# Kernel tuning notes

Measured on AMD Instinct MI355X. Metric: run time of the kernel, lower is better.

## Reference

```python
import jax, jax.numpy as jnp
import numpy as np

D_MODEL = 1024
HEAD = 16


def setup_inputs() -> dict:
    key = jax.random.key(0)
    ks = jax.random.split(key, 11)
    B, S, D = 2, 2048, D_MODEL
    s = 1.0 / np.sqrt(D)
    return {
        "query": jax.random.normal(ks[0], (B, S, D), jnp.float32),
        "value": jax.random.normal(ks[1], (B, S, D), jnp.float32),
        "key": jax.random.normal(ks[2], (B, S, D), jnp.float32),
        "Wq_w": jax.random.normal(ks[3], (D, D), jnp.float32) * s,
        "Wq_b": jnp.zeros((D,), jnp.float32),
        "Wk_w": jax.random.normal(ks[4], (D, D), jnp.float32) * s,
        "Wk_b": jnp.zeros((D,), jnp.float32),
        "Wv_w": jax.random.normal(ks[5], (D, D), jnp.float32) * s,
        "Wv_b": jnp.zeros((D,), jnp.float32),
        "Wo_w": jax.random.normal(ks[6], (D, D), jnp.float32) * s,
        "Wo_b": jnp.zeros((D,), jnp.float32),
    }


def reference(query, value, key, Wq_w, Wq_b, Wk_w, Wk_b, Wv_w, Wv_b, Wo_w, Wo_b):
    B, S, D = query.shape
    H = HEAD
    kd = D // H
    # Linear projections (torch Linear: x @ W.T + b)
    Q = query @ Wq_w.T + Wq_b
    K = key @ Wk_w.T + Wk_b
    V = value @ Wv_w.T + Wv_b
    # [B, S, D] -> [B, H, S, kd]
    Q = Q.reshape(B, S, H, kd).transpose(0, 2, 1, 3)
    K = K.reshape(B, S, H, kd).transpose(0, 2, 1, 3)
    V = V.reshape(B, S, H, kd).transpose(0, 2, 1, 3)
    scale = 1.0 / jnp.sqrt(jnp.asarray(kd, query.dtype))
    score = jnp.einsum("bhqd,bhkd->bhqk", Q, K) * scale  # [B,H,S,S]
    attn = jax.nn.softmax(score, axis=-1)
    x = jnp.einsum("bhqk,bhkd->bhqd", attn, V)  # [B,H,S,kd]
    x = x.transpose(0, 2, 1, 3).reshape(B, S, D)
    return x @ Wo_w.T + Wo_b
```

## Files before the change

kernel.cpp:

```cpp
#include <hip/hip_runtime.h>
#include <stdint.h>
#include <stddef.h>


typedef __attribute__((ext_vector_type(8))) short short8;
typedef __attribute__((ext_vector_type(4))) float floatx4;
typedef __attribute__((ext_vector_type(16))) float f32x16;
typedef __attribute__((ext_vector_type(4))) unsigned short ushort4v;

#define MFMA16(a, b, c) __builtin_amdgcn_mfma_f32_16x16x32_bf16((a), (b), (c), 0, 0, 0)
#define MFMA32(a, b, c) __builtin_amdgcn_mfma_f32_32x32x16_bf16((a), (b), (c), 0, 0, 0)

#define CL2 0.18033688011112042f

__device__ __forceinline__ unsigned short f2bf(float f) {
  union { float f; unsigned u; } v; v.f = f;
  unsigned u = v.u;
  return (unsigned short)((u + 0x7fffu + ((u >> 16) & 1u)) >> 16);
}

__device__ __forceinline__ float fast_exp2(float x) {
  float r;
  asm("v_exp_f32 %0, %1" : "=v"(r) : "v"(x));
  return r;
}

__device__ __forceinline__ unsigned cvt_pk_bf16(float lo, float hi) {
  unsigned r;
  asm("v_cvt_pk_bf16_f32 %0, %1, %2" : "=v"(r) : "v"(lo), "v"(hi));
  return r;
}

#define PSWAP(a, b) asm("v_permlane32_swap_b32 %0, %1" : "+v"(a), "+v"(b))

union B8 { unsigned short s[8]; short8 v; };
union U4 { unsigned w[4]; short8 v; };

__device__ __forceinline__ void gload_lds16(const unsigned short* g, unsigned short* l) {
  __builtin_amdgcn_global_load_lds(
      (__attribute__((address_space(1))) void*)(g),
      (__attribute__((address_space(3))) void*)(l), 16, 0, 0);
}

__global__ __launch_bounds__(256) void convert_all(
    const float* __restrict__ q, const float* __restrict__ k, const float* __restrict__ v,
    const float* __restrict__ wq, const float* __restrict__ wk,
    const float* __restrict__ wv, const float* __restrict__ wo,
    unsigned short* __restrict__ qb, unsigned short* __restrict__ kb,
    unsigned short* __restrict__ vb, unsigned short* __restrict__ w4)
{
  int b = blockIdx.x;
  const float* s; unsigned short* d;
  float sc = 1.0f;
  if (b < 2048)      { s = q;  d = qb; }
  else if (b < 4096) { s = k;  d = kb; b -= 2048; }
  else if (b < 6144) { s = v;  d = vb; b -= 4096; }
  else if (b < 6656) { s = wq; d = w4;            b -= 6144; sc = CL2; }
  else if (b < 7168) { s = wk; d = w4 + 1048576;  b -= 6656; }
  else if (b < 7680) { s = wv; d = w4 + 2097152;  b -= 7168; }
  else               { s = wo; d = w4 + 3145728;  b -= 7680; }
  const size_t i = ((size_t)b * 256 + threadIdx.x) * 8;
  float4 f0 = *(const float4*)(s + i);
  float4 f1 = *(const float4*)(s + i + 4);
  B8 u;
  u.s[0] = f2bf(f0.x * sc); u.s[1] = f2bf(f0.y * sc);
  u.s[2] = f2bf(f0.z * sc); u.s[3] = f2bf(f0.w * sc);
  u.s[4] = f2bf(f1.x * sc); u.s[5] = f2bf(f1.y * sc);
  u.s[6] = f2bf(f1.z * sc); u.s[7] = f2bf(f1.w * sc);
  *(short8*)(d + i) = u.v;
}

__global__ __launch_bounds__(256) void proj_gemm(
    const unsigned short* __restrict__ A0, const unsigned short* __restrict__ A1,
    const unsigned short* __restrict__ A2, const unsigned short* __restrict__ W4,
    const float* __restrict__ b0, const float* __restrict__ b1, const float* __restrict__ b2,
    unsigned short* __restrict__ Qp, unsigned short* __restrict__ Kp,
    unsigned short* __restrict__ Vt)
{
  const int z = blockIdx.z;
  const unsigned short* A = (z == 0) ? A0 : ((z == 1) ? A1 : A2);
  const unsigned short* W = W4 + (size_t)z * 1048576;
  const float* bias = (z == 0) ? b0 : ((z == 1) ? b1 : b2);
  const float esc = (z == 0) ? CL2 : 1.0f;

  const int m0 = blockIdx.y * 128;
  const int n0 = blockIdx.x * 128;
  const int tid = threadIdx.x;
  const int lane = tid & 63;
  const int wid = tid >> 6;
  const int wr = wid >> 1, wc = wid & 1;
  const int g = lane >> 4, l15 = lane & 15;

  __shared__ unsigned short As[2][128 * 32];
  __shared__ unsigned short Bs[2][128 * 32];

  const floatx4 vzero = {0.f, 0.f, 0.f, 0.f};
  floatx4 acc[4][4];
#pragma unroll
  for (int i = 0; i < 4; ++i)
#pragma unroll
    for (int j = 0; j < 4; ++j) acc[i][j] = vzero;

  const int lr = lane >> 2;
  const int lc = (lane & 3) * 8;
  const unsigned short* pa = &A[(size_t)(m0 + lr) * 1024 + lc];
  const unsigned short* pw = &W[(size_t)(n0 + lr) * 1024 + lc];

#pragma unroll
  for (int t = 0; t < 2; ++t) {
    const int rb = (t * 4 + wid) * 16;
    gload_lds16(pa + (size_t)rb * 1024, &As[0][rb * 32]);
    gload_lds16(pw + (size_t)rb * 1024, &Bs[0][rb * 32]);
  }
  __syncthreads();

  int cur = 0;
  for (int k0 = 0; k0 < 1024; k0 += 32) {
    if (k0 + 32 < 1024) {
#pragma unroll
      for (int t = 0; t < 2; ++t) {
        const int rb = (t * 4 + wid) * 16;
        gload_lds16(pa + (size_t)rb * 1024 + k0 + 32, &As[cur ^ 1][rb * 32]);
        gload_lds16(pw + (size_t)rb * 1024 + k0 + 32, &Bs[cur ^ 1][rb * 32]);
      }
    }

    short8 af[4], bfr[4];
#pragma unroll
    for (int mt = 0; mt < 4; ++mt)
      af[mt] = *(const short8*)&As[cur][(wr * 64 + mt * 16 + l15) * 32 + g * 8];
#pragma unroll
    for (int nt = 0; nt < 4; ++nt)
      bfr[nt] = *(const short8*)&Bs[cur][(wc * 64 + nt * 16 + l15) * 32 + g * 8];

    __builtin_amdgcn_s_setprio(1);
#pragma unroll
    for (int mt = 0; mt < 4; ++mt)
#pragma unroll
      for (int nt = 0; nt < 4; ++nt)
        acc[mt][nt] = MFMA16(af[mt], bfr[nt], acc[mt][nt]);
    __builtin_amdgcn_s_setprio(0);

    __syncthreads();
    cur ^= 1;
  }

  float bvv[4];
#pragma unroll
  for (int nt = 0; nt < 4; ++nt) bvv[nt] = bias[n0 + wc * 64 + nt * 16 + l15] * esc;

  if (z < 2) {
    unsigned short* dst = (z == 0) ? Qp : Kp;
#pragma unroll
    for (int mt = 0; mt < 4; ++mt)
#pragma unroll
      for (int r = 0; r < 4; ++r) {
        const size_t row = (size_t)(m0 + wr * 64 + mt * 16 + g * 4 + r);
#pragma unroll
        for (int nt = 0; nt < 4; ++nt)
          dst[row * 1024 + n0 + wc * 64 + nt * 16 + l15] =
              f2bf(acc[mt][nt][r] + bvv[nt]);
      }
  } else {
#pragma unroll
    for (int mt = 0; mt < 4; ++mt) {
      const int sr = m0 + wr * 64 + mt * 16 + g * 4;
      const int bb = sr >> 11;
      const int ss = sr & 2047;
#pragma unroll
      for (int nt = 0; nt < 4; ++nt) {
        const int n = n0 + wc * 64 + nt * 16 + l15;
        const int hh = n >> 6, dd = n & 63;
        ushort4v o;
#pragma unroll
        for (int r = 0; r < 4; ++r) o[r] = f2bf(acc[mt][nt][r] + bvv[nt]);
        *(ushort4v*)&Vt[((size_t)(bb * 16 + hh) * 64 + dd) * 2048 + ss] = o;
      }
    }
  }
}

__global__ __launch_bounds__(256) void attn_kernel(
    const unsigned short* __restrict__ Qp, const unsigned short* __restrict__ Kp,
    const unsigned short* __restrict__ Vt, unsigned short* __restrict__ X)
{
  const int qb = blockIdx.x;
  const int bh = blockIdx.y;
  const int b = bh >> 4, h = bh & 15;
  const int tid = threadIdx.x, lane = tid & 63, w = tid >> 6;
  const int l31 = lane & 31, hi = lane >> 5;

  __shared__ unsigned short KV[2][2][4096];

  const int qrow = b * 2048 + qb * 128 + w * 32 + l31;
  short8 Qf[4];
#pragma unroll
  for (int ks = 0; ks < 4; ++ks)
    Qf[ks] = *(const short8*)&Qp[(size_t)qrow * 1024 + h * 64 + ks * 16 + hi * 8];

  const int s0 = tid, s1 = tid + 256;
  const int r0 = s0 >> 3, g0 = (s0 & 7) ^ (r0 & 7);
  const int r1 = s1 >> 3, g1 = (s1 & 7) ^ (r1 & 7);
  const unsigned short* kq0 = Kp + (size_t)(b * 2048 + r0) * 1024 + h * 64 + g0 * 8;
  const unsigned short* kq1 = Kp + (size_t)(b * 2048 + r1) * 1024 + h * 64 + g1 * 8;
  const unsigned short* vq0 = Vt + (size_t)(bh * 64 + r0) * 2048 + g0 * 8;
  const unsigned short* vq1 = Vt + (size_t)(bh * 64 + r1) * 2048 + g1 * 8;
  const int db0 = (w * 64) * 8;
  const int db1 = (256 + w * 64) * 8;

  f32x16 o0, o1;
#pragma unroll
  for (int i = 0; i < 16; ++i) { o0[i] = 0.f; o1[i] = 0.f; }
  float l_run = 0.f;

  gload_lds16(kq0, &KV[0][0][db0]);
  gload_lds16(kq1, &KV[0][0][db1]);
  gload_lds16(vq0, &KV[0][1][db0]);
  gload_lds16(vq1, &KV[0][1][db1]);
  __syncthreads();

  int cur = 0;
  for (int t = 0; t < 32; ++t) {
    if (t + 1 < 32) {
      const size_t ko = (size_t)(t + 1) * 65536;
      const size_t vo = (size_t)(t + 1) * 64;
      gload_lds16(kq0 + ko, &KV[cur ^ 1][0][db0]);
      gload_lds16(kq1 + ko, &KV[cur ^ 1][0][db1]);
      gload_lds16(vq0 + vo, &KV[cur ^ 1][1][db0]);
      gload_lds16(vq1 + vo, &KV[cur ^ 1][1][db1]);
    }
    const unsigned short* Kb = &KV[cur][0][0];
    const unsigned short* Vb = &KV[cur][1][0];

    f32x16 c0, c1;
#pragma unroll
    for (int i = 0; i < 16; ++i) { c0[i] = 0.f; c1[i] = 0.f; }
    __builtin_amdgcn_s_setprio(1);
    {
      const int base = l31 * 64, kx = l31 & 7;
#pragma unroll
      for (int ks = 0; ks < 4; ++ks) {
        const short8 kf = *(const short8*)&Kb[base + (((ks * 2 + hi) ^ kx) << 3)];
        c0 = MFMA32(kf, Qf[ks], c0);
      }
    }
    {
      const int krow = 32 + l31;
      const int base = krow * 64, kx = krow & 7;
#pragma unroll
      for (int ks = 0; ks < 4; ++ks) {
        const short8 kf = *(const short8*)&Kb[base + (((ks * 2 + hi) ^ kx) << 3)];
        c1 = MFMA32(kf, Qf[ks], c1);
      }
    }
    __builtin_amdgcn_s_setprio(0);

    short8 vf0[4], vf1[4];
#pragma unroll
    for (int ks = 0; ks < 4; ++ks) {
      const int vx0 = l31 & 7;
      vf0[ks] = *(const short8*)&Vb[l31 * 64 + (((ks * 2 + hi) ^ vx0) << 3)];
      const int vrow = 32 + l31;
      vf1[ks] = *(const short8*)&Vb[vrow * 64 + (((ks * 2 + hi) ^ (vrow & 7)) << 3)];
    }

#pragma unroll
    for (int i = 0; i < 16; ++i) { c0[i] = fast_exp2(c0[i]); l_run += c0[i]; }
#pragma unroll
    for (int i = 0; i < 16; ++i) { c1[i] = fast_exp2(c1[i]); l_run += c1[i]; }

    short8 PA0, PA1, PA2, PA3;
    {
      unsigned p0 = cvt_pk_bf16(c0[0], c0[1]),   p1 = cvt_pk_bf16(c0[2], c0[3]);
      unsigned p2 = cvt_pk_bf16(c0[4], c0[5]),   p3 = cvt_pk_bf16(c0[6], c0[7]);
      unsigned p4 = cvt_pk_bf16(c0[8], c0[9]),   p5 = cvt_pk_bf16(c0[10], c0[11]);
      unsigned p6 = cvt_pk_bf16(c0[12], c0[13]), p7 = cvt_pk_bf16(c0[14], c0[15]);
      PSWAP(p0, p2); PSWAP(p1, p3); PSWAP(p4, p6); PSWAP(p5, p7);
      U4 a, bb_;
      a.w[0] = p0; a.w[1] = p1; a.w[2] = p2; a.w[3] = p3;          PA0 = a.v;
      bb_.w[0] = p4; bb_.w[1] = p5; bb_.w[2] = p6; bb_.w[3] = p7;  PA1 = bb_.v;
    }
    {
      unsigned p0 = cvt_pk_bf16(c1[0], c1[1]),   p1 = cvt_pk_bf16(c1[2], c1[3]);
      unsigned p2 = cvt_pk_bf16(c1[4], c1[5]),   p3 = cvt_pk_bf16(c1[6], c1[7]);
      unsigned p4 = cvt_pk_bf16(c1[8], c1[9]),   p5 = cvt_pk_bf16(c1[10], c1[11]);
      unsigned p6 = cvt_pk_bf16(c1[12], c1[13]), p7 = cvt_pk_bf16(c1[14], c1[15]);
      PSWAP(p0, p2); PSWAP(p1, p3); PSWAP(p4, p6); PSWAP(p5, p7);
      U4 a, bb_;
      a.w[0] = p0; a.w[1] = p1; a.w[2] = p2; a.w[3] = p3;          PA2 = a.v;
      bb_.w[0] = p4; bb_.w[1] = p5; bb_.w[2] = p6; bb_.w[3] = p7;  PA3 = bb_.v;
    }

    __builtin_amdgcn_s_setprio(1);
#pragma unroll
    for (int ks = 0; ks < 4; ++ks) {
      const short8 pa = (ks == 0) ? PA0 : (ks == 1) ? PA1 : (ks == 2) ? PA2 : PA3;
      o0 = MFMA32(vf0[ks], pa, o0);
      o1 = MFMA32(vf1[ks], pa, o1);
    }
    __builtin_amdgcn_s_setprio(0);

    __syncthreads();
    cur ^= 1;
  }

  const float l_tot = l_run + __shfl_xor(l_run, 32);
  const float linv = 1.f / l_tot;
#pragma unroll
  for (int a = 0; a < 4; ++a) {
    ushort4v v0, v1;
#pragma unroll
    for (int r = 0; r < 4; ++r) {
      v0[r] = f2bf(o0[a * 4 + r] * linv);
      v1[r] = f2bf(o1[a * 4 + r] * linv);
    }
    *(ushort4v*)&X[(size_t)qrow * 1024 + h * 64 + a * 8 + hi * 4] = v0;
    *(ushort4v*)&X[(size_t)qrow * 1024 + h * 64 + 32 + a * 8 + hi * 4] = v1;
  }
}

__global__ __launch_bounds__(256) void out_gemm(
    const unsigned short* __restrict__ A, const unsigned short* __restrict__ W,
    const float* __restrict__ bias, float* __restrict__ out)
{
  const int m0 = blockIdx.y * 64;
  const int n0 = blockIdx.x * 128;
  const int tid = threadIdx.x;
  const int lane = tid & 63;
  const int wid = tid >> 6;
  const int wr = wid >> 1, wc = wid & 1;
  const int g = lane >> 4, l15 = lane & 15;

  __shared__ unsigned short As[2][64 * 32];
  __shared__ unsigned short Bs[2][128 * 32];

  const floatx4 vzero = {0.f, 0.f, 0.f, 0.f};
  floatx4 acc[2][4];
#pragma unroll
  for (int i = 0; i < 2; ++i)
#pragma unroll
    for (int j = 0; j < 4; ++j) acc[i][j] = vzero;

  const int lr = lane >> 2;
  const int lc = (lane & 3) * 8;
  const unsigned short* pa = &A[(size_t)(m0 + lr) * 1024 + lc];
  const unsigned short* pw = &W[(size_t)(n0 + lr) * 1024 + lc];

#pragma unroll
  for (int t = 0; t < 2; ++t) {
    const int rb = (t * 4 + wid) * 16;
    gload_lds16(pw + (size_t)rb * 1024, &Bs[0][rb * 32]);
  }
  gload_lds16(pa + (size_t)(wid * 16) * 1024, &As[0][wid * 16 * 32]);
  __syncthreads();

  int cur = 0;
  for (int k0 = 0; k0 < 1024; k0 += 32) {
    if (k0 + 32 < 1024) {
#pragma unroll
      for (int t = 0; t < 2; ++t) {
        const int rb = (t * 4 + wid) * 16;
        gload_lds16(pw + (size_t)rb * 1024 + k0 + 32, &Bs[cur ^ 1][rb * 32]);
      }
      gload_lds16(pa + (size_t)(wid * 16) * 1024 + k0 + 32, &As[cur ^ 1][wid * 16 * 32]);
    }

    short8 af[2], bfr[4];
#pragma unroll
    for (int mt = 0; mt < 2; ++mt)
      af[mt] = *(const short8*)&As[cur][(wr * 32 + mt * 16 + l15) * 32 + g * 8];
#pragma unroll
    for (int nt = 0; nt < 4; ++nt)
      bfr[nt] = *(const short8*)&Bs[cur][(wc * 64 + nt * 16 + l15) * 32 + g * 8];

    __builtin_amdgcn_s_setprio(1);
#pragma unroll
    for (int mt = 0; mt < 2; ++mt)
#pragma unroll
      for (int nt = 0; nt < 4; ++nt)
        acc[mt][nt] = MFMA16(af[mt], bfr[nt], acc[mt][nt]);
    __builtin_amdgcn_s_setprio(0);

    __syncthreads();
    cur ^= 1;
  }

  float bvv[4];
#pragma unroll
  for (int nt = 0; nt < 4; ++nt) bvv[nt] = bias[n0 + wc * 64 + nt * 16 + l15];

#pragma unroll
  for (int mt = 0; mt < 2; ++mt)
#pragma unroll
    for (int r = 0; r < 4; ++r) {
      const size_t row = (size_t)(m0 + wr * 32 + mt * 16 + g * 4 + r);
#pragma unroll
      for (int nt = 0; nt < 4; ++nt)
        out[row * 1024 + n0 + wc * 64 + nt * 16 + l15] = acc[mt][nt][r] + bvv[nt];
    }
}

extern "C" void kernel_launch(void* const* d_in, const int* in_sizes, int n_in,
                              void* d_out, int out_size, void* d_ws, size_t ws_size,
                              hipStream_t stream)
{
  const float* query = (const float*)d_in[0];
  const float* value = (const float*)d_in[1];
  const float* key   = (const float*)d_in[2];
  const float* Wq = (const float*)d_in[3];
  const float* bq = (const float*)d_in[4];
  const float* Wk = (const float*)d_in[5];
  const float* bk = (const float*)d_in[6];
  const float* Wv = (const float*)d_in[7];
  const float* bv = (const float*)d_in[8];
  const float* Wo = (const float*)d_in[9];
  const float* bo = (const float*)d_in[10];
  float* out = (float*)d_out;

  const size_t M4 = (size_t)4096 * 1024;
  unsigned short* vb = (unsigned short*)d_ws;
  unsigned short* w4 = vb + M4;
  unsigned short* Qp = w4 + M4;
  unsigned short* Kp = Qp + M4;
  unsigned short* Vt = Kp + M4;
  unsigned short* X  = vb;
  unsigned short* qb = (unsigned short*)d_out;
  unsigned short* kb = qb + M4;

  dim3 blk(256);
  convert_all<<<8192, blk, 0, stream>>>(query, key, value, Wq, Wk, Wv, Wo,
                                        qb, kb, vb, w4);
  proj_gemm<<<dim3(8, 32, 3), blk, 0, stream>>>(qb, kb, vb, w4,
                                                bq, bk, bv, Qp, Kp, Vt);
  attn_kernel<<<dim3(16, 32), blk, 0, stream>>>(Qp, Kp, Vt, X);
  out_gemm<<<dim3(8, 64), blk, 0, stream>>>(X, w4 + 3 * 1048576, bo, out);
}
```

Measured before the change: 126.2 us.

## Split attention over two key halves and merge partials in a combine kernel

The attention kernel gains a grid z dimension of 2, so each block handles only half of the key/value tiles. Each block writes unnormalized bf16 partial outputs and per-row softmax denominators to scratch buffers. A new combine kernel sums the two partials and divides by the summed denominators to produce X. This doubles the number of attention blocks so the GPU has more parallel work, at the cost of an extra launch, extra global traffic and an added bf16 rounding of the unnormalized partials.

```diff
diff --git a/kernel.cpp b/kernel.cpp
--- a/kernel.cpp
+++ b/kernel.cpp
@@ -182,10 +182,13 @@
 
 __global__ __launch_bounds__(256) void attn_kernel(
     const unsigned short* __restrict__ Qp, const unsigned short* __restrict__ Kp,
-    const unsigned short* __restrict__ Vt, unsigned short* __restrict__ X)
+    const unsigned short* __restrict__ Vt,
+    unsigned short* __restrict__ O0, unsigned short* __restrict__ O1,
+    float* __restrict__ lp)
 {
   const int qb = blockIdx.x;
   const int bh = blockIdx.y;
+  const int z = blockIdx.z;
   const int b = bh >> 4, h = bh & 15;
   const int tid = threadIdx.x, lane = tid & 63, w = tid >> 6;
   const int l31 = lane & 31, hi = lane >> 5;
@@ -213,15 +216,17 @@
   for (int i = 0; i < 16; ++i) { o0[i] = 0.f; o1[i] = 0.f; }
   float l_run = 0.f;
 
-  gload_lds16(kq0, &KV[0][0][db0]);
-  gload_lds16(kq1, &KV[0][0][db1]);
-  gload_lds16(vq0, &KV[0][1][db0]);
-  gload_lds16(vq1, &KV[0][1][db1]);
+  const int t0 = z * 16, t1 = t0 + 16;
+
+  gload_lds16(kq0 + (size_t)t0 * 65536, &KV[0][0][db0]);
+  gload_lds16(kq1 + (size_t)t0 * 65536, &KV[0][0][db1]);
+  gload_lds16(vq0 + (size_t)t0 * 64,    &KV[0][1][db0]);
+  gload_lds16(vq1 + (size_t)t0 * 64,    &KV[0][1][db1]);
   __syncthreads();
 
   int cur = 0;
-  for (int t = 0; t < 32; ++t) {
-    if (t + 1 < 32) {
+  for (int t = t0; t < t1; ++t) {
+    if (t + 1 < t1) {
       const size_t ko = (size_t)(t + 1) * 65536;
       const size_t vo = (size_t)(t + 1) * 64;
       gload_lds16(kq0 + ko, &KV[cur ^ 1][0][db0]);
@@ -305,18 +310,40 @@
   }
 
   const float l_tot = l_run + __shfl_xor(l_run, 32);
-  const float linv = 1.f / l_tot;
+  unsigned short* Op = z ? O1 : O0;
+  if (!hi) lp[(z * 16 + h) * 4096 + qrow] = l_tot;
 #pragma unroll
   for (int a = 0; a < 4; ++a) {
     ushort4v v0, v1;
 #pragma unroll
     for (int r = 0; r < 4; ++r) {
-      v0[r] = f2bf(o0[a * 4 + r] * linv);
-      v1[r] = f2bf(o1[a * 4 + r] * linv);
-    }
-    *(ushort4v*)&X[(size_t)qrow * 1024 + h * 64 + a * 8 + hi * 4] = v0;
-    *(ushort4v*)&X[(size_t)qrow * 1024 + h * 64 + 32 + a * 8 + hi * 4] = v1;
-  }
+      v0[r] = f2bf(o0[a * 4 + r]);
+      v1[r] = f2bf(o1[a * 4 + r]);
+    }
+    *(ushort4v*)&Op[(size_t)qrow * 1024 + h * 64 + a * 8 + hi * 4] = v0;
+    *(ushort4v*)&Op[(size_t)qrow * 1024 + h * 64 + 32 + a * 8 + hi * 4] = v1;
+  }
+}
+
+__global__ __launch_bounds__(256) void combine_kernel(
+    const unsigned short* __restrict__ O0, const unsigned short* __restrict__ O1,
+    const float* __restrict__ lp, unsigned short* __restrict__ X)
+{
+  const size_t e = ((size_t)blockIdx.x * 256 + threadIdx.x) * 8;
+  const int qrow = (int)(e >> 10);
+  const int h = ((int)e & 1023) >> 6;
+  const float inv = 1.f / (lp[h * 4096 + qrow] + lp[(16 + h) * 4096 + qrow]);
+  B8 ua, ub, o;
+  ua.v = *(const short8*)(O0 + e);
+  ub.v = *(const short8*)(O1 + e);
+#pragma unroll
+  for (int j = 0; j < 8; ++j) {
+    union { unsigned u; float f; } fa, fb;
+    fa.u = ((unsigned)ua.s[j]) << 16;
+    fb.u = ((unsigned)ub.s[j]) << 16;
+    o.s[j] = f2bf((fa.f + fb.f) * inv);
+  }
+  *(short8*)(X + e) = o.v;
 }
 
 __global__ __launch_bounds__(256) void out_gemm(
@@ -423,15 +450,19 @@
   unsigned short* Qp = w4 + M4;
   unsigned short* Kp = Qp + M4;
   unsigned short* Vt = Kp + M4;
-  unsigned short* X  = vb;
   unsigned short* qb = (unsigned short*)d_out;
   unsigned short* kb = qb + M4;
+  unsigned short* O0 = vb;
+  unsigned short* O1 = (unsigned short*)d_out;
+  float* lp = (float*)((unsigned short*)d_out + M4);
+  unsigned short* X = vb;
 
   dim3 blk(256);
   convert_all<<<8192, blk, 0, stream>>>(query, key, value, Wq, Wk, Wv, Wo,
                                         qb, kb, vb, w4);
   proj_gemm<<<dim3(8, 32, 3), blk, 0, stream>>>(qb, kb, vb, w4,
                                                 bq, bk, bv, Qp, Kp, Vt);
-  attn_kernel<<<dim3(16, 32), blk, 0, stream>>>(Qp, Kp, Vt, X);
+  attn_kernel<<<dim3(16, 32, 2), blk, 0, stream>>>(Qp, Kp, Vt, O0, O1, lp);
+  combine_kernel<<<2048, blk, 0, stream>>>(O0, O1, lp, X);
   out_gemm<<<dim3(8, 64), blk, 0, stream>>>(X, w4 + 3 * 1048576, bo, out);
 }
```

Result: slower. 133.9 us (+6.1%).

## Use triple-buffered LDS pipelines with partial vmcnt waits in all kernels

Applied to the files above, without the earlier changes.

Replaces the double-buffered global-to-LDS prefetch in the QKV GEMM, attention and output GEMM kernels with a three-stage ring. Each iteration waits only on the older outstanding loads via s_waitcnt vmcnt(N) plus one barrier, instead of a full __syncthreads at the end, so two stages of loads stay in flight. The attention row-sum is also split into four partial accumulators to shorten the dependency chain. The cost is more LDS per block, which may lower occupancy, and the explicit vmcnt counts must match the number of loads issued per stage.

```diff
diff --git a/kernel.cpp b/kernel.cpp
--- a/kernel.cpp
+++ b/kernel.cpp
@@ -32,6 +32,12 @@
 }
 
 #define PSWAP(a, b) asm("v_permlane32_swap_b32 %0, %1" : "+v"(a), "+v"(b))
+
+#define WAITBAR(N) do { \
+  asm volatile("s_waitcnt vmcnt(" #N ")" ::: "memory"); \
+  __builtin_amdgcn_s_barrier(); \
+  __builtin_amdgcn_sched_barrier(0); \
+} while (0)
 
 union B8 { unsigned short s[8]; short8 v; };
 union U4 { unsigned w[4]; short8 v; };
@@ -91,8 +97,8 @@
   const int wr = wid >> 1, wc = wid & 1;
   const int g = lane >> 4, l15 = lane & 15;
 
-  __shared__ unsigned short As[2][128 * 32];
-  __shared__ unsigned short Bs[2][128 * 32];
+  __shared__ unsigned short As[3][128 * 32];
+  __shared__ unsigned short Bs[3][128 * 32];
 
   const floatx4 vzero = {0.f, 0.f, 0.f, 0.f};
   floatx4 acc[4][4];
@@ -105,24 +111,24 @@
   const int lc = (lane & 3) * 8;
   const unsigned short* pa = &A[(size_t)(m0 + lr) * 1024 + lc];
   const unsigned short* pw = &W[(size_t)(n0 + lr) * 1024 + lc];
-
-#pragma unroll
-  for (int t = 0; t < 2; ++t) {
-    const int rb = (t * 4 + wid) * 16;
-    gload_lds16(pa + (size_t)rb * 1024, &As[0][rb * 32]);
-    gload_lds16(pw + (size_t)rb * 1024, &Bs[0][rb * 32]);
-  }
-  __syncthreads();
+  const int rb0 = wid * 16, rb1 = (4 + wid) * 16;
+
+#define PSTAGE(s_, b_) do { \
+    gload_lds16(pa + (size_t)rb0 * 1024 + (s_) * 32, &As[b_][rb0 * 32]); \
+    gload_lds16(pa + (size_t)rb1 * 1024 + (s_) * 32, &As[b_][rb1 * 32]); \
+    gload_lds16(pw + (size_t)rb0 * 1024 + (s_) * 32, &Bs[b_][rb0 * 32]); \
+    gload_lds16(pw + (size_t)rb1 * 1024 + (s_) * 32, &Bs[b_][rb1 * 32]); \
+  } while (0)
+
+  PSTAGE(0, 0);
+  PSTAGE(1, 1);
 
   int cur = 0;
-  for (int k0 = 0; k0 < 1024; k0 += 32) {
-    if (k0 + 32 < 1024) {
-#pragma unroll
-      for (int t = 0; t < 2; ++t) {
-        const int rb = (t * 4 + wid) * 16;
-        gload_lds16(pa + (size_t)rb * 1024 + k0 + 32, &As[cur ^ 1][rb * 32]);
-        gload_lds16(pw + (size_t)rb * 1024 + k0 + 32, &Bs[cur ^ 1][rb * 32]);
-      }
+  for (int s = 0; s < 32; ++s) {
+    if (s < 31) WAITBAR(4); else WAITBAR(0);
+    if (s + 2 < 32) {
+      int nb = cur + 2; if (nb >= 3) nb -= 3;
+      PSTAGE(s + 2, nb);
     }
 
     short8 af[4], bfr[4];
@@ -141,9 +147,9 @@
         acc[mt][nt] = MFMA16(af[mt], bfr[nt], acc[mt][nt]);
     __builtin_amdgcn_s_setprio(0);
 
-    __syncthreads();
-    cur ^= 1;
+    cur = (cur + 1 == 3) ? 0 : cur + 1;
   }
+#undef PSTAGE
 
   float bvv[4];
 #pragma unroll
@@ -190,7 +196,7 @@
   const int tid = threadIdx.x, lane = tid & 63, w = tid >> 6;
   const int l31 = lane & 31, hi = lane >> 5;
 
-  __shared__ unsigned short KV[2][2][4096];
+  __shared__ unsigned short KV[3][2][4096];
 
   const int qrow = b * 2048 + qb * 128 + w * 32 + l31;
   short8 Qf[4];
@@ -208,26 +214,28 @@
   const int db0 = (w * 64) * 8;
   const int db1 = (256 + w * 64) * 8;
 
+#define ASTAGE(t_, b_) do { \
+    const size_t ko = (size_t)(t_) * 65536, vo = (size_t)(t_) * 64; \
+    gload_lds16(kq0 + ko, &KV[b_][0][db0]); \
+    gload_lds16(kq1 + ko, &KV[b_][0][db1]); \
+    gload_lds16(vq0 + vo, &KV[b_][1][db0]); \
+    gload_lds16(vq1 + vo, &KV[b_][1][db1]); \
+  } while (0)
+
   f32x16 o0, o1;
 #pragma unroll
   for (int i = 0; i < 16; ++i) { o0[i] = 0.f; o1[i] = 0.f; }
-  float l_run = 0.f;
-
-  gload_lds16(kq0, &KV[0][0][db0]);
-  gload_lds16(kq1, &KV[0][0][db1]);
-  gload_lds16(vq0, &KV[0][1][db0]);
-  gload_lds16(vq1, &KV[0][1][db1]);
-  __syncthreads();
+  float lp4[4] = {0.f, 0.f, 0.f, 0.f};
+
+  ASTAGE(0, 0);
+  ASTAGE(1, 1);
 
   int cur = 0;
   for (int t = 0; t < 32; ++t) {
-    if (t + 1 < 32) {
-      const size_t ko = (size_t)(t + 1) * 65536;
-      const size_t vo = (size_t)(t + 1) * 64;
-      gload_lds16(kq0 + ko, &KV[cur ^ 1][0][db0]);
-      gload_lds16(kq1 + ko, &KV[cur ^ 1][0][db1]);
-      gload_lds16(vq0 + vo, &KV[cur ^ 1][1][db0]);
-      gload_lds16(vq1 + vo, &KV[cur ^ 1][1][db1]);
+    if (t < 31) WAITBAR(4); else WAITBAR(0);
+    if (t + 2 < 32) {
+      int nb = cur + 2; if (nb >= 3) nb -= 3;
+      ASTAGE(t + 2, nb);
     }
     const unsigned short* Kb = &KV[cur][0][0];
     const unsigned short* Vb = &KV[cur][1][0];
@@ -265,9 +273,9 @@
     }
 
 #pragma unroll
-    for (int i = 0; i < 16; ++i) { c0[i] = fast_exp2(c0[i]); l_run += c0[i]; }
-#pragma unroll
-    for (int i = 0; i < 16; ++i) { c1[i] = fast_exp2(c1[i]); l_run += c1[i]; }
+    for (int i = 0; i < 16; ++i) { c0[i] = fast_exp2(c0[i]); lp4[i & 3] += c0[i]; }
+#pragma unroll
+    for (int i = 0; i < 16; ++i) { c1[i] = fast_exp2(c1[i]); lp4[i & 3] += c1[i]; }
 
     short8 PA0, PA1, PA2, PA3;
     {
@@ -300,10 +308,11 @@
     }
     __builtin_amdgcn_s_setprio(0);
 
-    __syncthreads();
-    cur ^= 1;
+    cur = (cur + 1 == 3) ? 0 : cur + 1;
   }
-
+#undef ASTAGE
+
+  const float l_run = (lp4[0] + lp4[1]) + (lp4[2] + lp4[3]);
   const float l_tot = l_run + __shfl_xor(l_run, 32);
   const float linv = 1.f / l_tot;
 #pragma unroll
@@ -331,8 +340,8 @@
   const int wr = wid >> 1, wc = wid & 1;
   const int g = lane >> 4, l15 = lane & 15;
 
-  __shared__ unsigned short As[2][64 * 32];
-  __shared__ unsigned short Bs[2][128 * 32];
+  __shared__ unsigned short As[3][64 * 32];
+  __shared__ unsigned short Bs[3][128 * 32];
 
   const floatx4 vzero = {0.f, 0.f, 0.f, 0.f};
   floatx4 acc[2][4];
@@ -345,24 +354,23 @@
   const int lc = (lane & 3) * 8;
   const unsigned short* pa = &A[(size_t)(m0 + lr) * 1024 + lc];
   const unsigned short* pw = &W[(size_t)(n0 + lr) * 1024 + lc];
-
-#pragma unroll
-  for (int t = 0; t < 2; ++t) {
-    const int rb = (t * 4 + wid) * 16;
-    gload_lds16(pw + (size_t)rb * 1024, &Bs[0][rb * 32]);
-  }
-  gload_lds16(pa + (size_t)(wid * 16) * 1024, &As[0][wid * 16 * 32]);
-  __syncthreads();
+  const int rb0 = wid * 16, rb1 = (4 + wid) * 16;
+
+#define OSTAGE(s_, b_) do { \
+    gload_lds16(pa + (size_t)rb0 * 1024 + (s_) * 32, &As[b_][rb0 * 32]); \
+    gload_lds16(pw + (size_t)rb0 * 1024 + (s_) * 32, &Bs[b_][rb0 * 32]); \
+    gload_lds16(pw + (size_t)rb1 * 1024 + (s_) * 32, &Bs[b_][rb1 * 32]); \
+  } while (0)
+
+  OSTAGE(0, 0);
+  OSTAGE(1, 1);
 
   int cur = 0;
-  for (int k0 = 0; k0 < 1024; k0 += 32) {
-    if (k0 + 32 < 1024) {
-#pragma unroll
-      for (int t = 0; t < 2; ++t) {
-        const int rb = (t * 4 + wid) * 16;
-        gload_lds16(pw + (size_t)rb * 1024 + k0 + 32, &Bs[cur ^ 1][rb * 32]);
-      }
-      gload_lds16(pa + (size_t)(wid * 16) * 1024 + k0 + 32, &As[cur ^ 1][wid * 16 * 32]);
+  for (int s = 0; s < 32; ++s) {
+    if (s < 31) WAITBAR(3); else WAITBAR(0);
+    if (s + 2 < 32) {
+      int nb = cur + 2; if (nb >= 3) nb -= 3;
+      OSTAGE(s + 2, nb);
     }
 
     short8 af[2], bfr[4];
@@ -381,9 +389,9 @@
         acc[mt][nt] = MFMA16(af[mt], bfr[nt], acc[mt][nt]);
     __builtin_amdgcn_s_setprio(0);
 
-    __syncthreads();
-    cur ^= 1;
+    cur = (cur + 1 == 3) ? 0 : cur + 1;
   }
+#undef OSTAGE
 
   float bvv[4];
 #pragma unroll
```

Result: slower. 130.5 us, median of 2 (+3.4%).
